# Kernel tuning notes

Measured on AMD Instinct MI355X. Metric: run time of the kernel, lower is better.

## Reference

```python
import jax, jax.numpy as jnp
import numpy as np

N = 50000      # nodes
E = 1600000    # edges
M = 2          # modalities
DIN, H1, LAT, DEC, HID, NC = 2000, 500, 128, 64, 64, 16
EPS = 1e-5


def setup_inputs() -> dict:
    key = jax.random.key(0)
    ks = jax.random.split(key, 24)
    s = 0.02
    return {
        "x": jax.random.normal(ks[0], (M, N, DIN), jnp.float32),
        "src": jax.random.randint(ks[1], (E,), 0, N, jnp.int32),
        "dst": jax.random.randint(ks[2], (E,), 0, N, jnp.int32),
        "W1": jax.random.normal(ks[3], (M, DIN, H1), jnp.float32) * s,
        "b1": jax.random.normal(ks[4], (M, H1), jnp.float32) * s,
        "g1": jax.random.uniform(ks[5], (M, H1), jnp.float32) + 0.5,
        "be1": jax.random.normal(ks[6], (M, H1), jnp.float32) * s,
        "m1": jax.random.normal(ks[7], (M, H1), jnp.float32) * s,
        "v1": jax.random.uniform(ks[8], (M, H1), jnp.float32) + 0.5,
        "W2": jax.random.normal(ks[9], (M, H1, LAT), jnp.float32) * s,
        "b2": jax.random.normal(ks[10], (M, LAT), jnp.float32) * s,
        "g2": jax.random.uniform(ks[11], (M, LAT), jnp.float32) + 0.5,
        "be2": jax.random.normal(ks[12], (M, LAT), jnp.float32) * s,
        "m2": jax.random.normal(ks[13], (M, LAT), jnp.float32) * s,
        "v2": jax.random.uniform(ks[14], (M, LAT), jnp.float32) + 0.5,
        "Wd": jax.random.normal(ks[15], (M, LAT, DEC), jnp.float32) * s,
        "bd": jax.random.normal(ks[16], (M, DEC), jnp.float32) * s,
        "Wg1": jax.random.normal(ks[17], (DEC, HID), jnp.float32) * s,
        "bg1": jax.random.normal(ks[18], (HID,), jnp.float32) * s,
        "Wg2": jax.random.normal(ks[19], (HID, NC), jnp.float32) * s,
        "bg2": jax.random.normal(ks[20], (NC,), jnp.float32) * s,
    }


def _bn(h, g, b, m, v):
    # inference-mode BatchNorm1d; params broadcast over [M, 1, F]
    return (h - m[:, None, :]) * jax.lax.rsqrt(v[:, None, :] + EPS) * g[:, None, :] + b[:, None, :]


def reference(x, src, dst, W1, b1, g1, be1, m1, v1, W2, b2, g2, be2, m2, v2,
              Wd, bd, Wg1, bg1, Wg2, bg2):
    # --- multi-modal encoders (dropout = identity at eval) ---
    h = jnp.einsum('mnd,mdh->mnh', x, W1) + b1[:, None, :]        # [M,N,500]
    h = _bn(h, g1, be1, m1, v1)
    h = jnp.einsum('mnh,mhl->mnl', h, W2) + b2[:, None, :]        # [M,N,LAT]
    h = _bn(h, g2, be2, m2, v2)
    dec = jnp.einsum('mnl,mld->mnd', h, Wd) + bd[:, None, :]      # [M,N,DEC]
    node_features = jnp.mean(dec, axis=0)                         # [N,DEC]

    # --- GraphConv (DGL norm='both'): D_out^{-1/2} on src, D_in^{-1/2} on dst ---
    ones = jnp.ones(src.shape[0], jnp.float32)
    deg_out = jax.ops.segment_sum(ones, src, num_segments=N)
    deg_in = jax.ops.segment_sum(ones, dst, num_segments=N)
    c_src = jax.lax.rsqrt(jnp.clip(deg_out, 1.0))[:, None]
    c_dst = jax.lax.rsqrt(jnp.clip(deg_in, 1.0))[:, None]

    def gconv(feat, W, b):
        msg = (feat * c_src)[src]                                 # [E,F]
        agg = jax.ops.segment_sum(msg, dst, num_segments=N)       # [N,F]
        return (agg * c_dst) @ W + b

    h = jax.nn.relu(gconv(node_features, Wg1, bg1))               # [N,HID]
    score = gconv(h, Wg2, bg2)                                    # [N,NC]
    return score
```

## Files before the change

kernel.cpp:

```cpp
#include <hip/hip_runtime.h>

#define NN 50000
#define EE 1600000
#define MM 2
#define DIN 2000
#define H1 500
#define LAT 128
#define DECF 64
#define KTOT (MM*DIN)
#define KSTEPS (KTOT/32)
#define EPSBN 1e-5f

typedef float f32x4 __attribute__((ext_vector_type(4)));
typedef short short8v __attribute__((ext_vector_type(8)));

__device__ __forceinline__ unsigned int pkbf(float a, float b){
  unsigned int ua = __float_as_uint(a), ub = __float_as_uint(b);
  ua = (ua + 0x7FFFu + ((ua>>16)&1u)) >> 16;
  ub = (ub + 0x7FFFu + ((ub>>16)&1u)) & 0xFFFF0000u;
  return ua | ub;
}

__global__ __launch_bounds__(256) void prepA(const float* __restrict__ W2,const float* __restrict__ Wd,
                      const float* __restrict__ g2,const float* __restrict__ v2,
                      float* __restrict__ T){
  __shared__ float a2[LAT];
  int m = (blockIdx.x*4) / H1;
  if (threadIdx.x < LAT)
    a2[threadIdx.x] = g2[m*LAT+threadIdx.x]*rsqrtf(v2[m*LAT+threadIdx.x]+EPSBN);
  __syncthreads();
  int g = blockIdx.x*256 + threadIdx.x;
  int d = g & 63; int mk = g >> 6; int k = mk % H1;
  const float* w2 = W2 + (size_t)(m*H1 + k)*LAT;
  const float* wd = Wd + (size_t)m*LAT*DECF + d;
  float acc = 0.f;
  for (int l = 0; l < LAT; ++l) acc += w2[l]*a2[l]*wd[(size_t)l*DECF];
  T[g] = acc;
}

__global__ __launch_bounds__(256) void prepB(const float* __restrict__ W1,const float* __restrict__ g1,
                      const float* __restrict__ v1,const float* __restrict__ T,
                      unsigned short* __restrict__ WB){
  __shared__ float a1[H1];
  int m = (blockIdx.x*4) / DIN;
  for (int k = threadIdx.x; k < H1; k += 256)
    a1[k] = g1[m*H1+k]*rsqrtf(v1[m*H1+k]+EPSBN);
  __syncthreads();
  int g = blockIdx.x*256 + threadIdx.x;
  int d = g & 63; int mi = g >> 6; int i = mi % DIN;
  const float* w1 = W1 + (size_t)(m*DIN + i)*H1;
  const float* t  = T + (size_t)m*H1*DECF + d;
  float acc = 0.f;
  for (int k = 0; k < H1; ++k) acc += w1[k]*a1[k]*t[(size_t)k*DECF];
  acc *= 0.5f;
  unsigned int u = __float_as_uint(acc);
  unsigned short bf = (unsigned short)((u + 0x7FFFu + ((u>>16)&1u)) >> 16);
  int kc = m*DIN + i;
  int s = kc >> 5, kl = kc & 31;
  int laneB = ((kl>>3)<<4) | (d & 15);
  int t4 = d >> 4;
  WB[((size_t)((s*4 + t4)*64 + laneB))*8 + (kl & 7)] = bf;
}

__global__ void prepC(const float* __restrict__ b1,const float* __restrict__ g1,const float* __restrict__ be1,
                      const float* __restrict__ m1,const float* __restrict__ v1,
                      const float* __restrict__ b2,const float* __restrict__ g2,const float* __restrict__ be2,
                      const float* __restrict__ m2,const float* __restrict__ v2,
                      const float* __restrict__ T,const float* __restrict__ Wd,
                      const float* __restrict__ bd, float* __restrict__ cbar){
  int d = threadIdx.x;
  if (d >= DECF) return;
  float s = 0.f;
  for (int m = 0; m < MM; ++m){
    float sm = bd[m*DECF + d];
    const float* t = T + (size_t)m*H1*DECF + d;
    for (int k = 0; k < H1; ++k){
      float a = g1[m*H1+k]*rsqrtf(v1[m*H1+k]+EPSBN);
      float c = (b1[m*H1+k]-m1[m*H1+k])*a + be1[m*H1+k];
      sm += c*t[(size_t)k*DECF];
    }
    const float* wd = Wd + (size_t)m*LAT*DECF + d;
    for (int l = 0; l < LAT; ++l){
      float a = g2[m*LAT+l]*rsqrtf(v2[m*LAT+l]+EPSBN);
      float c = (b2[m*LAT+l]-m2[m*LAT+l])*a + be2[m*LAT+l];
      sm += c*wd[(size_t)l*DECF];
    }
    s += sm;
  }
  cbar[d] = 0.5f*s;
}

__global__ void degk(const int* __restrict__ src,const int* __restrict__ dst,
                     int* __restrict__ dout,int* __restrict__ din){
  int e = blockIdx.x*blockDim.x + threadIdx.x;
  if (e >= EE) return;
  atomicAdd(&dout[src[e]], 1);
  atomicAdd(&din[dst[e]], 1);
}

__global__ __launch_bounds__(1024) void scan1(const int* __restrict__ deg, int* __restrict__ rp,
                      int* __restrict__ bsum, int n){
  __shared__ int sm[1024];
  int i = blockIdx.x*1024 + threadIdx.x;
  int v = (i < n) ? deg[i] : 0;
  sm[threadIdx.x] = v; __syncthreads();
  for (int off=1; off<1024; off<<=1){
    int t = (threadIdx.x >= off) ? sm[threadIdx.x-off] : 0;
    __syncthreads();
    sm[threadIdx.x] += t;
    __syncthreads();
  }
  if (i < n) rp[i] = sm[threadIdx.x] - v;
  if (threadIdx.x == 1023) bsum[blockIdx.x] = sm[1023];
}

__global__ void scan3n(int* __restrict__ rp, const int* __restrict__ bsum,
                       const int* __restrict__ dout, const int* __restrict__ din,
                       float* __restrict__ csrc, float* __restrict__ cdst){
  int i = blockIdx.x*blockDim.x + threadIdx.x;
  if (i >= NN) return;
  int b = i >> 10;
  int base = 0;
  for (int j = 0; j < b; ++j) base += bsum[j];
  rp[i] += base;
  if (i == NN-1) rp[NN] = EE;
  int a = dout[i]; if (a < 1) a = 1;
  int dd = din[i]; if (dd < 1) dd = 1;
  csrc[i] = rsqrtf((float)a);
  cdst[i] = rsqrtf((float)dd);
}

__global__ void scatk(const int* __restrict__ src,const int* __restrict__ dst,
                      const int* __restrict__ rp,int* __restrict__ cur,int* __restrict__ ss){
  int e = blockIdx.x*blockDim.x + threadIdx.x;
  if (e >= EE) return;
  int d = dst[e];
  int p = rp[d] + atomicAdd(&cur[d], 1);
  ss[p] = src[e];
}

__global__ __launch_bounds__(256) void gemm_nf(
    const float* __restrict__ x, const short8v* __restrict__ WB,
    const float* __restrict__ cbar, const float* __restrict__ csrc,
    float* __restrict__ nfpre)
{
  const int lane = threadIdx.x & 63;
  const int wave = threadIdx.x >> 6;
  const int n0 = blockIdx.x*64 + wave*16;
  const int r = lane & 15;
  const int kg = (lane >> 4) << 3;
  int row = n0 + r; if (row > NN-1) row = NN-1;
  const float* xrow = x + (size_t)row * DIN;

  f32x4 acc0 = {0.f,0.f,0.f,0.f}, acc1 = acc0, acc2 = acc0, acc3 = acc0;

  f32x4 A0c, A1c; short8v B0c, B1c, B2c, B3c;
  {
    const float* p = xrow + kg;
    A0c = *(const f32x4*)p; A1c = *(const f32x4*)(p+4);
    const short8v* bp = WB + lane;
    B0c = bp[0]; B1c = bp[64]; B2c = bp[128]; B3c = bp[192];
  }
  for (int s = 0; s < KSTEPS-1; ++s){
    f32x4 A0n, A1n; short8v B0n, B1n, B2n, B3n;
    {
      int kr = (s+1)*32 + kg;
      const float* p = (kr < DIN) ? (xrow + kr)
                                  : (xrow + (size_t)(NN-1)*DIN + kr);
      A0n = *(const f32x4*)p; A1n = *(const f32x4*)(p+4);
      const short8v* bp = WB + (size_t)(s+1)*256 + lane;
      B0n = bp[0]; B1n = bp[64]; B2n = bp[128]; B3n = bp[192];
    }
    union { short8v v; unsigned int u[4]; } AF;
    AF.u[0]=pkbf(A0c[0],A0c[1]); AF.u[1]=pkbf(A0c[2],A0c[3]);
    AF.u[2]=pkbf(A1c[0],A1c[1]); AF.u[3]=pkbf(A1c[2],A1c[3]);
    acc0 = __builtin_amdgcn_mfma_f32_16x16x32_bf16(AF.v, B0c, acc0, 0,0,0);
    acc1 = __builtin_amdgcn_mfma_f32_16x16x32_bf16(AF.v, B1c, acc1, 0,0,0);
    acc2 = __builtin_amdgcn_mfma_f32_16x16x32_bf16(AF.v, B2c, acc2, 0,0,0);
    acc3 = __builtin_amdgcn_mfma_f32_16x16x32_bf16(AF.v, B3c, acc3, 0,0,0);
    A0c=A0n; A1c=A1n; B0c=B0n; B1c=B1n; B2c=B2n; B3c=B3n;
  }
  {
    union { short8v v; unsigned int u[4]; } AF;
    AF.u[0]=pkbf(A0c[0],A0c[1]); AF.u[1]=pkbf(A0c[2],A0c[3]);
    AF.u[2]=pkbf(A1c[0],A1c[1]); AF.u[3]=pkbf(A1c[2],A1c[3]);
    acc0 = __builtin_amdgcn_mfma_f32_16x16x32_bf16(AF.v, B0c, acc0, 0,0,0);
    acc1 = __builtin_amdgcn_mfma_f32_16x16x32_bf16(AF.v, B1c, acc1, 0,0,0);
    acc2 = __builtin_amdgcn_mfma_f32_16x16x32_bf16(AF.v, B2c, acc2, 0,0,0);
    acc3 = __builtin_amdgcn_mfma_f32_16x16x32_bf16(AF.v, B3c, acc3, 0,0,0);
  }
  const int rg = (lane >> 4) << 2;
  float cb0 = cbar[r], cb1 = cbar[16+r], cb2 = cbar[32+r], cb3 = cbar[48+r];
  #pragma unroll
  for (int rr = 0; rr < 4; ++rr){
    int rowD = n0 + rg + rr;
    if (rowD < NN){
      float cs = csrc[rowD];
      float* o = nfpre + (size_t)rowD*64 + r;
      o[0]  = (acc0[rr] + cb0)*cs;
      o[16] = (acc1[rr] + cb1)*cs;
      o[32] = (acc2[rr] + cb2)*cs;
      o[48] = (acc3[rr] + cb3)*cs;
    }
  }
}

__global__ __launch_bounds__(256) void fgd1(const float* __restrict__ nf,const int* __restrict__ rp,
                      const int* __restrict__ ss,const float* __restrict__ Wg1,
                      const float* __restrict__ bg1,const float* __restrict__ csrc,
                      const float* __restrict__ cdst,float* __restrict__ hpre){
  __shared__ float W[64*64];
  for (int i = threadIdx.x; i < 64*64; i += 256) W[i] = Wg1[i];
  __syncthreads();
  int wave = threadIdx.x >> 6, lane = threadIdx.x & 63;
  int n = blockIdx.x*4 + wave;
  if (n >= NN) return;
  int q = lane >> 4, c0 = (lane & 15)*4;
  int beg = rp[n], end = rp[n+1];
  f32x4 s4 = {0.f,0.f,0.f,0.f};
  int e = beg + q;
  for (; e + 4 < end; e += 8){
    int i0 = ss[e], i1 = ss[e+4];
    f32x4 f0 = *(const f32x4*)(nf + (size_t)i0*64 + c0);
    f32x4 f1 = *(const f32x4*)(nf + (size_t)i1*64 + c0);
    s4 += f0 + f1;
  }
  if (e < end)
    s4 += *(const f32x4*)(nf + (size_t)ss[e]*64 + c0);
  s4.x += __shfl_xor(s4.x,16); s4.y += __shfl_xor(s4.y,16);
  s4.z += __shfl_xor(s4.z,16); s4.w += __shfl_xor(s4.w,16);
  s4.x += __shfl_xor(s4.x,32); s4.y += __shfl_xor(s4.y,32);
  s4.z += __shfl_xor(s4.z,32); s4.w += __shfl_xor(s4.w,32);
  float acc = 0.f;
  #pragma unroll
  for (int l16 = 0; l16 < 16; ++l16){
    acc += __shfl(s4.x,l16) * W[(4*l16+0)*64 + lane];
    acc += __shfl(s4.y,l16) * W[(4*l16+1)*64 + lane];
    acc += __shfl(s4.z,l16) * W[(4*l16+2)*64 + lane];
    acc += __shfl(s4.w,l16) * W[(4*l16+3)*64 + lane];
  }
  float h = fmaxf(cdst[n]*acc + bg1[lane], 0.f) * csrc[n];
  hpre[(size_t)n*64 + lane] = h;
}

__global__ __launch_bounds__(256) void fgd2(const float* __restrict__ hp,const int* __restrict__ rp,
                      const int* __restrict__ ss,const float* __restrict__ Wg2,
                      const float* __restrict__ bg2,const float* __restrict__ cdst,
                      float* __restrict__ score){
  __shared__ float W[64*16];
  for (int i = threadIdx.x; i < 64*16; i += 256) W[i] = Wg2[i];
  __syncthreads();
  int wave = threadIdx.x >> 6, lane = threadIdx.x & 63;
  int n = blockIdx.x*4 + wave;
  if (n >= NN) return;
  int q = lane >> 4, c0 = (lane & 15)*4;
  int beg = rp[n], end = rp[n+1];
  f32x4 s4 = {0.f,0.f,0.f,0.f};
  int e = beg + q;
  for (; e + 4 < end; e += 8){
    int i0 = ss[e], i1 = ss[e+4];
    f32x4 f0 = *(const f32x4*)(hp + (size_t)i0*64 + c0);
    f32x4 f1 = *(const f32x4*)(hp + (size_t)i1*64 + c0);
    s4 += f0 + f1;
  }
  if (e < end)
    s4 += *(const f32x4*)(hp + (size_t)ss[e]*64 + c0);
  s4.x += __shfl_xor(s4.x,16); s4.y += __shfl_xor(s4.y,16);
  s4.z += __shfl_xor(s4.z,16); s4.w += __shfl_xor(s4.w,16);
  s4.x += __shfl_xor(s4.x,32); s4.y += __shfl_xor(s4.y,32);
  s4.z += __shfl_xor(s4.z,32); s4.w += __shfl_xor(s4.w,32);
  int c = lane & 15;
  float acc = 0.f;
  #pragma unroll
  for (int l16 = 0; l16 < 16; ++l16){
    acc += __shfl(s4.x,l16) * W[(4*l16+0)*16 + c];
    acc += __shfl(s4.y,l16) * W[(4*l16+1)*16 + c];
    acc += __shfl(s4.z,l16) * W[(4*l16+2)*16 + c];
    acc += __shfl(s4.w,l16) * W[(4*l16+3)*16 + c];
  }
  if (lane < 16) score[(size_t)n*16 + lane] = cdst[n]*acc + bg2[lane];
}

extern "C" void kernel_launch(void* const* d_in, const int* in_sizes, int n_in,
                              void* d_out, int out_size, void* d_ws, size_t ws_size,
                              hipStream_t stream){
  const float* x   = (const float*)d_in[0];
  const int* src   = (const int*)d_in[1];
  const int* dst   = (const int*)d_in[2];
  const float* W1  = (const float*)d_in[3];
  const float* b1  = (const float*)d_in[4];
  const float* g1  = (const float*)d_in[5];
  const float* be1 = (const float*)d_in[6];
  const float* m1  = (const float*)d_in[7];
  const float* v1  = (const float*)d_in[8];
  const float* W2  = (const float*)d_in[9];
  const float* b2  = (const float*)d_in[10];
  const float* g2  = (const float*)d_in[11];
  const float* be2 = (const float*)d_in[12];
  const float* m2  = (const float*)d_in[13];
  const float* v2  = (const float*)d_in[14];
  const float* Wd  = (const float*)d_in[15];
  const float* bd  = (const float*)d_in[16];
  const float* Wg1 = (const float*)d_in[17];
  const float* bg1 = (const float*)d_in[18];
  const float* Wg2 = (const float*)d_in[19];
  const float* bg2 = (const float*)d_in[20];
  float* score = (float*)d_out;

  char* w = (char*)d_ws;
  size_t off = 0;
  auto alc = [&](size_t b){ size_t c = off; off += (b + 255) & ~(size_t)255; return c; };
  size_t o_dout = alc((size_t)NN*4), o_din = alc((size_t)NN*4), o_cur = alc((size_t)NN*4);
  size_t zspan = off;
  size_t o_rp  = alc((size_t)(NN+1)*4), o_bsum = alc(256*4);
  size_t o_csrc = alc((size_t)NN*4), o_cdst = alc((size_t)NN*4);
  size_t o_T = alc((size_t)MM*H1*DECF*4), o_cbar = alc(DECF*4);
  size_t o_WB = alc((size_t)MM*DIN*DECF*2);
  size_t o_ss = alc((size_t)EE*4);
  size_t o_nf = alc((size_t)NN*64*4);
  size_t o_hp = alc((size_t)NN*64*4);

  int* dout = (int*)(w+o_dout); int* din = (int*)(w+o_din); int* cur = (int*)(w+o_cur);
  int* rp = (int*)(w+o_rp); int* bsum = (int*)(w+o_bsum);
  float* csrc = (float*)(w+o_csrc); float* cdst = (float*)(w+o_cdst);
  float* T = (float*)(w+o_T); float* cbar = (float*)(w+o_cbar);
  unsigned short* WBu = (unsigned short*)(w+o_WB);
  int* ss = (int*)(w+o_ss);
  float* nf = (float*)(w+o_nf); float* hp = (float*)(w+o_hp);

  hipMemsetAsync(w, 0, zspan, stream);

  prepA<<<(MM*H1*DECF)/256,256,0,stream>>>(W2,Wd,g2,v2,T);
  prepB<<<(MM*DIN*DECF)/256,256,0,stream>>>(W1,g1,v1,T,WBu);
  prepC<<<1,64,0,stream>>>(b1,g1,be1,m1,v1,b2,g2,be2,m2,v2,T,Wd,bd,cbar);

  degk<<<(EE+255)/256,256,0,stream>>>(src,dst,dout,din);
  int nb = (NN+1023)/1024;
  scan1<<<nb,1024,0,stream>>>(din,rp,bsum,NN);
  scan3n<<<(NN+255)/256,256,0,stream>>>(rp,bsum,dout,din,csrc,cdst);
  scatk<<<(EE+255)/256,256,0,stream>>>(src,dst,rp,cur,ss);

  gemm_nf<<<(NN+63)/64,256,0,stream>>>(x,(const short8v*)(w+o_WB),cbar,csrc,nf);

  fgd1<<<(NN+3)/4,256,0,stream>>>(nf,rp,ss,Wg1,bg1,csrc,cdst,hp);
  fgd2<<<(NN+3)/4,256,0,stream>>>(hp,rp,ss,Wg2,bg2,cdst,score);
}
```

Before: 857.7 us.

## Use persistent atomic-ticket GEMM, wider gather unroll, and split prepC reduction

The node-feature GEMM becomes a persistent kernel with 768 blocks. Each wave grabs 16-row tiles from an atomic ticket counter, which replaces the one-shot grid and is meant to balance load and cut tail effects. The two graph aggregation kernels now use 512-thread blocks, unroll the neighbor gather to 4 loads per iteration and drop their bounds checks, relying on NN being divisible by 8. prepC splits its reduction across two thread halves and combines them through shared memory. The ticket adds atomic traffic, and the tile bounds check is removed on the assumption that NN is a multiple of 16.

```diff
diff --git a/kernel.cpp b/kernel.cpp
--- a/kernel.cpp
+++ b/kernel.cpp
@@ -9,6 +9,7 @@
 #define DECF 64
 #define KTOT (MM*DIN)
 #define KSTEPS (KTOT/32)
+#define NTILES (NN/16)
 #define EPSBN 1e-5f
 
 typedef float f32x4 __attribute__((ext_vector_type(4)));
@@ -68,26 +69,27 @@
                       const float* __restrict__ m2,const float* __restrict__ v2,
                       const float* __restrict__ T,const float* __restrict__ Wd,
                       const float* __restrict__ bd, float* __restrict__ cbar){
-  int d = threadIdx.x;
-  if (d >= DECF) return;
+  __shared__ float part[128];
+  int d = threadIdx.x & 63, h = threadIdx.x >> 6;
   float s = 0.f;
   for (int m = 0; m < MM; ++m){
-    float sm = bd[m*DECF + d];
+    if (h == 0) s += bd[m*DECF + d];
     const float* t = T + (size_t)m*H1*DECF + d;
-    for (int k = 0; k < H1; ++k){
+    for (int k = h*(H1/2); k < (h+1)*(H1/2); ++k){
       float a = g1[m*H1+k]*rsqrtf(v1[m*H1+k]+EPSBN);
       float c = (b1[m*H1+k]-m1[m*H1+k])*a + be1[m*H1+k];
-      sm += c*t[(size_t)k*DECF];
+      s += c*t[(size_t)k*DECF];
     }
     const float* wd = Wd + (size_t)m*LAT*DECF + d;
-    for (int l = 0; l < LAT; ++l){
+    for (int l = h*(LAT/2); l < (h+1)*(LAT/2); ++l){
       float a = g2[m*LAT+l]*rsqrtf(v2[m*LAT+l]+EPSBN);
       float c = (b2[m*LAT+l]-m2[m*LAT+l])*a + be2[m*LAT+l];
-      sm += c*wd[(size_t)l*DECF];
-    }
-    s += sm;
-  }
-  cbar[d] = 0.5f*s;
+      s += c*wd[(size_t)l*DECF];
+    }
+  }
+  part[threadIdx.x] = s;
+  __syncthreads();
+  if (h == 0) cbar[d] = 0.5f*(part[d] + part[64+d]);
 }
 
 __global__ void degk(const int* __restrict__ src,const int* __restrict__ dst,
@@ -142,59 +144,61 @@
 __global__ __launch_bounds__(256) void gemm_nf(
     const float* __restrict__ x, const short8v* __restrict__ WB,
     const float* __restrict__ cbar, const float* __restrict__ csrc,
-    float* __restrict__ nfpre)
+    float* __restrict__ nfpre, int* __restrict__ ticket)
 {
   const int lane = threadIdx.x & 63;
-  const int wave = threadIdx.x >> 6;
-  const int n0 = blockIdx.x*64 + wave*16;
   const int r = lane & 15;
   const int kg = (lane >> 4) << 3;
-  int row = n0 + r; if (row > NN-1) row = NN-1;
-  const float* xrow = x + (size_t)row * DIN;
-
-  f32x4 acc0 = {0.f,0.f,0.f,0.f}, acc1 = acc0, acc2 = acc0, acc3 = acc0;
-
-  f32x4 A0c, A1c; short8v B0c, B1c, B2c, B3c;
-  {
-    const float* p = xrow + kg;
-    A0c = *(const f32x4*)p; A1c = *(const f32x4*)(p+4);
-    const short8v* bp = WB + lane;
-    B0c = bp[0]; B1c = bp[64]; B2c = bp[128]; B3c = bp[192];
-  }
-  for (int s = 0; s < KSTEPS-1; ++s){
-    f32x4 A0n, A1n; short8v B0n, B1n, B2n, B3n;
+  const int rg = (lane >> 4) << 2;
+  const float cb0 = cbar[r], cb1 = cbar[16+r], cb2 = cbar[32+r], cb3 = cbar[48+r];
+
+  while (true){
+    int t = 0;
+    if (lane == 0) t = atomicAdd(ticket, 1);
+    t = __shfl(t, 0, 64);
+    if (t >= NTILES) break;
+    const int n0 = t*16;
+    const float* xrow = x + (size_t)(n0 + r) * DIN;
+
+    f32x4 acc0 = {0.f,0.f,0.f,0.f}, acc1 = acc0, acc2 = acc0, acc3 = acc0;
+    f32x4 A0c, A1c; short8v B0c, B1c, B2c, B3c;
     {
-      int kr = (s+1)*32 + kg;
-      const float* p = (kr < DIN) ? (xrow + kr)
-                                  : (xrow + (size_t)(NN-1)*DIN + kr);
-      A0n = *(const f32x4*)p; A1n = *(const f32x4*)(p+4);
-      const short8v* bp = WB + (size_t)(s+1)*256 + lane;
-      B0n = bp[0]; B1n = bp[64]; B2n = bp[128]; B3n = bp[192];
-    }
-    union { short8v v; unsigned int u[4]; } AF;
-    AF.u[0]=pkbf(A0c[0],A0c[1]); AF.u[1]=pkbf(A0c[2],A0c[3]);
-    AF.u[2]=pkbf(A1c[0],A1c[1]); AF.u[3]=pkbf(A1c[2],A1c[3]);
-    acc0 = __builtin_amdgcn_mfma_f32_16x16x32_bf16(AF.v, B0c, acc0, 0,0,0);
-    acc1 = __builtin_amdgcn_mfma_f32_16x16x32_bf16(AF.v, B1c, acc1, 0,0,0);
-    acc2 = __builtin_amdgcn_mfma_f32_16x16x32_bf16(AF.v, B2c, acc2, 0,0,0);
-    acc3 = __builtin_amdgcn_mfma_f32_16x16x32_bf16(AF.v, B3c, acc3, 0,0,0);
-    A0c=A0n; A1c=A1n; B0c=B0n; B1c=B1n; B2c=B2n; B3c=B3n;
-  }
-  {
-    union { short8v v; unsigned int u[4]; } AF;
-    AF.u[0]=pkbf(A0c[0],A0c[1]); AF.u[1]=pkbf(A0c[2],A0c[3]);
-    AF.u[2]=pkbf(A1c[0],A1c[1]); AF.u[3]=pkbf(A1c[2],A1c[3]);
-    acc0 = __builtin_amdgcn_mfma_f32_16x16x32_bf16(AF.v, B0c, acc0, 0,0,0);
-    acc1 = __builtin_amdgcn_mfma_f32_16x16x32_bf16(AF.v, B1c, acc1, 0,0,0);
-    acc2 = __builtin_amdgcn_mfma_f32_16x16x32_bf16(AF.v, B2c, acc2, 0,0,0);
-    acc3 = __builtin_amdgcn_mfma_f32_16x16x32_bf16(AF.v, B3c, acc3, 0,0,0);
-  }
-  const int rg = (lane >> 4) << 2;
-  float cb0 = cbar[r], cb1 = cbar[16+r], cb2 = cbar[32+r], cb3 = cbar[48+r];
-  #pragma unroll
-  for (int rr = 0; rr < 4; ++rr){
-    int rowD = n0 + rg + rr;
-    if (rowD < NN){
+      const float* p = xrow + kg;
+      A0c = *(const f32x4*)p; A1c = *(const f32x4*)(p+4);
+      const short8v* bp = WB + lane;
+      B0c = bp[0]; B1c = bp[64]; B2c = bp[128]; B3c = bp[192];
+    }
+    for (int s = 0; s < KSTEPS-1; ++s){
+      f32x4 A0n, A1n; short8v B0n, B1n, B2n, B3n;
+      {
+        int kr = (s+1)*32 + kg;
+        const float* p = (kr < DIN) ? (xrow + kr)
+                                    : (xrow + (size_t)(NN-1)*DIN + kr);
+        A0n = *(const f32x4*)p; A1n = *(const f32x4*)(p+4);
+        const short8v* bp = WB + (size_t)(s+1)*256 + lane;
+        B0n = bp[0]; B1n = bp[64]; B2n = bp[128]; B3n = bp[192];
+      }
+      union { short8v v; unsigned int u[4]; } AF;
+      AF.u[0]=pkbf(A0c[0],A0c[1]); AF.u[1]=pkbf(A0c[2],A0c[3]);
+      AF.u[2]=pkbf(A1c[0],A1c[1]); AF.u[3]=pkbf(A1c[2],A1c[3]);
+      acc0 = __builtin_amdgcn_mfma_f32_16x16x32_bf16(AF.v, B0c, acc0, 0,0,0);
+      acc1 = __builtin_amdgcn_mfma_f32_16x16x32_bf16(AF.v, B1c, acc1, 0,0,0);
+      acc2 = __builtin_amdgcn_mfma_f32_16x16x32_bf16(AF.v, B2c, acc2, 0,0,0);
+      acc3 = __builtin_amdgcn_mfma_f32_16x16x32_bf16(AF.v, B3c, acc3, 0,0,0);
+      A0c=A0n; A1c=A1n; B0c=B0n; B1c=B1n; B2c=B2n; B3c=B3n;
+    }
+    {
+      union { short8v v; unsigned int u[4]; } AF;
+      AF.u[0]=pkbf(A0c[0],A0c[1]); AF.u[1]=pkbf(A0c[2],A0c[3]);
+      AF.u[2]=pkbf(A1c[0],A1c[1]); AF.u[3]=pkbf(A1c[2],A1c[3]);
+      acc0 = __builtin_amdgcn_mfma_f32_16x16x32_bf16(AF.v, B0c, acc0, 0,0,0);
+      acc1 = __builtin_amdgcn_mfma_f32_16x16x32_bf16(AF.v, B1c, acc1, 0,0,0);
+      acc2 = __builtin_amdgcn_mfma_f32_16x16x32_bf16(AF.v, B2c, acc2, 0,0,0);
+      acc3 = __builtin_amdgcn_mfma_f32_16x16x32_bf16(AF.v, B3c, acc3, 0,0,0);
+    }
+    #pragma unroll
+    for (int rr = 0; rr < 4; ++rr){
+      int rowD = n0 + rg + rr;
       float cs = csrc[rowD];
       float* o = nfpre + (size_t)rowD*64 + r;
       o[0]  = (acc0[rr] + cb0)*cs;
@@ -205,27 +209,28 @@
   }
 }
 
-__global__ __launch_bounds__(256) void fgd1(const float* __restrict__ nf,const int* __restrict__ rp,
+__global__ __launch_bounds__(512) void fgd1(const float* __restrict__ nf,const int* __restrict__ rp,
                       const int* __restrict__ ss,const float* __restrict__ Wg1,
                       const float* __restrict__ bg1,const float* __restrict__ csrc,
                       const float* __restrict__ cdst,float* __restrict__ hpre){
   __shared__ float W[64*64];
-  for (int i = threadIdx.x; i < 64*64; i += 256) W[i] = Wg1[i];
+  for (int i = threadIdx.x; i < 64*64; i += 512) W[i] = Wg1[i];
   __syncthreads();
   int wave = threadIdx.x >> 6, lane = threadIdx.x & 63;
-  int n = blockIdx.x*4 + wave;
-  if (n >= NN) return;
+  int n = blockIdx.x*8 + wave;
   int q = lane >> 4, c0 = (lane & 15)*4;
   int beg = rp[n], end = rp[n+1];
   f32x4 s4 = {0.f,0.f,0.f,0.f};
   int e = beg + q;
-  for (; e + 4 < end; e += 8){
-    int i0 = ss[e], i1 = ss[e+4];
+  for (; e + 12 < end; e += 16){
+    int i0 = ss[e], i1 = ss[e+4], i2 = ss[e+8], i3 = ss[e+12];
     f32x4 f0 = *(const f32x4*)(nf + (size_t)i0*64 + c0);
     f32x4 f1 = *(const f32x4*)(nf + (size_t)i1*64 + c0);
-    s4 += f0 + f1;
-  }
-  if (e < end)
+    f32x4 f2 = *(const f32x4*)(nf + (size_t)i2*64 + c0);
+    f32x4 f3 = *(const f32x4*)(nf + (size_t)i3*64 + c0);
+    s4 += (f0 + f1) + (f2 + f3);
+  }
+  for (; e < end; e += 4)
     s4 += *(const f32x4*)(nf + (size_t)ss[e]*64 + c0);
   s4.x += __shfl_xor(s4.x,16); s4.y += __shfl_xor(s4.y,16);
   s4.z += __shfl_xor(s4.z,16); s4.w += __shfl_xor(s4.w,16);
@@ -243,27 +248,28 @@
   hpre[(size_t)n*64 + lane] = h;
 }
 
-__global__ __launch_bounds__(256) void fgd2(const float* __restrict__ hp,const int* __restrict__ rp,
+__global__ __launch_bounds__(512) void fgd2(const float* __restrict__ hp,const int* __restrict__ rp,
                       const int* __restrict__ ss,const float* __restrict__ Wg2,
                       const float* __restrict__ bg2,const float* __restrict__ cdst,
                       float* __restrict__ score){
   __shared__ float W[64*16];
-  for (int i = threadIdx.x; i < 64*16; i += 256) W[i] = Wg2[i];
+  for (int i = threadIdx.x; i < 64*16; i += 512) W[i] = Wg2[i];
   __syncthreads();
   int wave = threadIdx.x >> 6, lane = threadIdx.x & 63;
-  int n = blockIdx.x*4 + wave;
-  if (n >= NN) return;
+  int n = blockIdx.x*8 + wave;
   int q = lane >> 4, c0 = (lane & 15)*4;
   int beg = rp[n], end = rp[n+1];
   f32x4 s4 = {0.f,0.f,0.f,0.f};
   int e = beg + q;
-  for (; e + 4 < end; e += 8){
-    int i0 = ss[e], i1 = ss[e+4];
+  for (; e + 12 < end; e += 16){
+    int i0 = ss[e], i1 = ss[e+4], i2 = ss[e+8], i3 = ss[e+12];
     f32x4 f0 = *(const f32x4*)(hp + (size_t)i0*64 + c0);
     f32x4 f1 = *(const f32x4*)(hp + (size_t)i1*64 + c0);
-    s4 += f0 + f1;
-  }
-  if (e < end)
+    f32x4 f2 = *(const f32x4*)(hp + (size_t)i2*64 + c0);
+    f32x4 f3 = *(const f32x4*)(hp + (size_t)i3*64 + c0);
+    s4 += (f0 + f1) + (f2 + f3);
+  }
+  for (; e < end; e += 4)
     s4 += *(const f32x4*)(hp + (size_t)ss[e]*64 + c0);
   s4.x += __shfl_xor(s4.x,16); s4.y += __shfl_xor(s4.y,16);
   s4.z += __shfl_xor(s4.z,16); s4.w += __shfl_xor(s4.w,16);
@@ -311,6 +317,7 @@
   size_t off = 0;
   auto alc = [&](size_t b){ size_t c = off; off += (b + 255) & ~(size_t)255; return c; };
   size_t o_dout = alc((size_t)NN*4), o_din = alc((size_t)NN*4), o_cur = alc((size_t)NN*4);
+  size_t o_tick = alc(256);
   size_t zspan = off;
   size_t o_rp  = alc((size_t)(NN+1)*4), o_bsum = alc(256*4);
   size_t o_csrc = alc((size_t)NN*4), o_cdst = alc((size_t)NN*4);
@@ -321,6 +328,7 @@
   size_t o_hp = alc((size_t)NN*64*4);
 
   int* dout = (int*)(w+o_dout); int* din = (int*)(w+o_din); int* cur = (int*)(w+o_cur);
+  int* tick = (int*)(w+o_tick);
   int* rp = (int*)(w+o_rp); int* bsum = (int*)(w+o_bsum);
   float* csrc = (float*)(w+o_csrc); float* cdst = (float*)(w+o_cdst);
   float* T = (float*)(w+o_T); float* cbar = (float*)(w+o_cbar);
@@ -332,7 +340,7 @@
 
   prepA<<<(MM*H1*DECF)/256,256,0,stream>>>(W2,Wd,g2,v2,T);
   prepB<<<(MM*DIN*DECF)/256,256,0,stream>>>(W1,g1,v1,T,WBu);
-  prepC<<<1,64,0,stream>>>(b1,g1,be1,m1,v1,b2,g2,be2,m2,v2,T,Wd,bd,cbar);
+  prepC<<<1,128,0,stream>>>(b1,g1,be1,m1,v1,b2,g2,be2,m2,v2,T,Wd,bd,cbar);
 
   degk<<<(EE+255)/256,256,0,stream>>>(src,dst,dout,din);
   int nb = (NN+1023)/1024;
@@ -340,8 +348,8 @@
   scan3n<<<(NN+255)/256,256,0,stream>>>(rp,bsum,dout,din,csrc,cdst);
   scatk<<<(EE+255)/256,256,0,stream>>>(src,dst,rp,cur,ss);
 
-  gemm_nf<<<(NN+63)/64,256,0,stream>>>(x,(const short8v*)(w+o_WB),cbar,csrc,nf);
-
-  fgd1<<<(NN+3)/4,256,0,stream>>>(nf,rp,ss,Wg1,bg1,csrc,cdst,hp);
-  fgd2<<<(NN+3)/4,256,0,stream>>>(hp,rp,ss,Wg2,bg2,cdst,score);
-}
+  gemm_nf<<<768,256,0,stream>>>(x,(const short8v*)(w+o_WB),cbar,csrc,nf,tick);
+
+  fgd1<<<NN/8,512,0,stream>>>(nf,rp,ss,Wg1,bg1,csrc,cdst,hp);
+  fgd2<<<NN/8,512,0,stream>>>(hp,rp,ss,Wg2,bg2,cdst,score);
+}
```

New measurement: 797.4 us. 1.08x faster.
